# Optimization experiments

Measured on AMD Instinct MI355X. Metric: run time of the kernel, lower is better.

The kernel has to match this reference:

```python
import jax, jax.numpy as jnp
import numpy as np

B, N, D, H = 4, 4096, 64, 128
N_STATES = 6
K = 10  # top-k nearest neighbors in detect_basins
EPS = 1e-12


def setup_inputs() -> dict:
    key = jax.random.key(0)
    ks = jax.random.split(key, 12)
    s = 0.05
    return {
        "conformations": jax.random.normal(ks[0], (B, N, D), dtype=jnp.float32),
        "native_state": jax.random.normal(ks[1], (B, D), dtype=jnp.float32),
        # energy net: D -> H -> H//2 -> 1
        "We1": jax.random.normal(ks[2], (D, H), dtype=jnp.float32) * s,
        "be1": jnp.zeros((H,), jnp.float32),
        "We2": jax.random.normal(ks[3], (H, H // 2), dtype=jnp.float32) * s,
        "be2": jnp.zeros((H // 2,), jnp.float32),
        "We3": jax.random.normal(ks[4], (H // 2, 1), dtype=jnp.float32) * s,
        "be3": jnp.zeros((1,), jnp.float32),
        # state classifier: D -> H -> 6
        "Ws1": jax.random.normal(ks[5], (D, H), dtype=jnp.float32) * s,
        "bs1": jnp.zeros((H,), jnp.float32),
        "Ws2": jax.random.normal(ks[6], (H, N_STATES), dtype=jnp.float32) * s,
        "bs2": jnp.zeros((N_STATES,), jnp.float32),
    }


def reference(conformations, native_state, We1, be1, We2, be2, We3, be3, Ws1, bs1, Ws2, bs2):
    relu = jax.nn.relu

    def analyze(conf, native):  # conf: (N, D), native: (D,)
        # predict_energy
        h = relu(conf @ We1 + be1)
        h = relu(h @ We2 + be2)
        e = (h @ We3 + be3)[:, 0]  # (N,)

        # detect_basins: pairwise euclidean distances via Gram trick
        sq = jnp.sum(conf * conf, axis=-1)  # (N,)
        d2 = sq[:, None] + sq[None, :] - 2.0 * (conf @ conf.T)
        dist = jnp.sqrt(jnp.clip(d2, EPS))  # (N, N); eps keeps sqrt grad finite at diag

        negv, idx = jax.lax.top_k(-dist, K)   # ascending distances; idx[:,0] == self
        r = -negv[:, -1]                      # k-th smallest distance per row
        neigh_e = e[idx[:, 1:]]               # (N, K-1) energies of 9 nearest neighbors
        is_basin = jnp.all(e[:, None] <= neigh_e, axis=1)  # local-minimum test

        mask = dist < r[:, None]              # points strictly inside basin radius (incl self)
        depth = jnp.max(jnp.where(mask, e[None, :], -jnp.inf), axis=1) - e
        width = jnp.sum(jnp.where(mask, dist, 0.0), axis=1) / jnp.sum(mask, axis=1)

        # classify_state (computed for every sample; original queries it per basin center)
        logits = relu(conf @ Ws1 + bs1) @ Ws2 + bs2  # (N, 6)

        # compute_funnel_metrics
        nd = jnp.sqrt(jnp.sum((conf - native) ** 2, axis=-1))  # (N,)
        native_energy = e[jnp.argmin(nd)]
        funnel_depth = jnp.max(e) - native_energy
        ruggedness = jnp.std(e, ddof=1)  # torch.std is unbiased
        corr = jnp.corrcoef(jnp.stack([nd, e]))[0, 1]
        se = e[jnp.argsort(nd)]
        frustration = jnp.mean((se[1:] > se[:-1]).astype(jnp.float32))
        metrics = jnp.stack([funnel_depth, ruggedness, corr, frustration, native_energy])
        return e, is_basin, depth, width, logits, metrics

    return jax.vmap(analyze)(conformations, native_state)
```

## Files before the change

kernel.cpp:

```cpp
#include <hip/hip_runtime.h>
#include <float.h>
#include <math.h>

#define NPTS 4096
#define NBATCH 4
#define BN (NBATCH * NPTS)
#define EPSC 1e-12f
#define JS 4
#define CSTRIDE 204
#define NT (NPTS / JS / 64)

typedef __attribute__((ext_vector_type(8))) short bfrag;
typedef __attribute__((ext_vector_type(4))) short bhalf;
typedef __attribute__((ext_vector_type(4))) float f32x4;

#define MFMA(A, B, C) __builtin_amdgcn_mfma_f32_16x16x32_bf16((A), (B), (C), 0, 0, 0)

__device__ __forceinline__ bool dless(float d1, int i1, float d2, int i2) {
  return (d1 < d2) || ((d1 == d2) && (i1 < i2));
}

__device__ __forceinline__ unsigned short f2bf(float x) {
  unsigned b = __float_as_uint(x);
  return (unsigned short)((b + 0x7FFFu + ((b >> 16) & 1u)) >> 16);
}
__device__ __forceinline__ float bf2f(unsigned short u) {
  return __uint_as_float(((unsigned)u) << 16);
}
__device__ __forceinline__ void bf3(float x, unsigned short& u0, unsigned short& u1,
                                    unsigned short& u2) {
  u0 = f2bf(x);
  float r = x - bf2f(u0);
  u1 = f2bf(r);
  r = r - bf2f(u1);
  u2 = f2bf(r);
}

__device__ __forceinline__ void cp16(const void* g, void* l) {
  __builtin_amdgcn_global_load_lds(
      (const __attribute__((address_space(1))) unsigned int*)g,
      (__attribute__((address_space(3))) unsigned int*)l, 16, 0, 0);
}
__device__ __forceinline__ void cp4(const void* g, void* l) {
  __builtin_amdgcn_global_load_lds(
      (const __attribute__((address_space(1))) unsigned int*)g,
      (__attribute__((address_space(3))) unsigned int*)l, 4, 0, 0);
}

__device__ __forceinline__ void gemm32x128(const float (*A)[64], const float* W,
                                           const float* bias, float (*O)[128], int tid) {
  const int pi = (tid >> 5) << 2;
  const int ci = (tid & 31) << 2;
  float acc[4][4] = {};
  for (int k0 = 0; k0 < 64; k0 += 4) {
    alignas(16) float av[4][4], wv[4][4];
#pragma unroll
    for (int r = 0; r < 4; ++r) *(float4*)av[r] = *(const float4*)&A[pi + r][k0];
#pragma unroll
    for (int kk = 0; kk < 4; ++kk) *(float4*)wv[kk] = *(const float4*)&W[(k0 + kk) * 128 + ci];
#pragma unroll
    for (int kk = 0; kk < 4; ++kk)
#pragma unroll
      for (int r = 0; r < 4; ++r)
#pragma unroll
        for (int c = 0; c < 4; ++c)
          acc[r][c] = fmaf(av[r][kk], wv[kk][c], acc[r][c]);
  }
#pragma unroll
  for (int r = 0; r < 4; ++r)
#pragma unroll
    for (int c = 0; c < 4; ++c)
      O[pi + r][ci + c] = fmaxf(acc[r][c] + bias[ci + c], 0.f);
}

__global__ __launch_bounds__(256) void mlp_kernel(
    const float* __restrict__ conf, const float* __restrict__ native,
    const float* __restrict__ We1, const float* __restrict__ be1,
    const float* __restrict__ We2, const float* __restrict__ be2,
    const float* __restrict__ We3, const float* __restrict__ be3,
    const float* __restrict__ Ws1, const float* __restrict__ bs1,
    const float* __restrict__ Ws2, const float* __restrict__ bs2,
    float* __restrict__ e_out, float* __restrict__ logits_out,
    float* __restrict__ sq_ws, float* __restrict__ nd_ws,
    unsigned short* __restrict__ cbf) {
  __shared__ __align__(16) float Wbuf[8192];
  __shared__ __align__(16) float confs[32][64];
  __shared__ __align__(16) float hbuf[32][128];
  __shared__ float nat[64];
  __shared__ float b1s[128], b2s[64], w3s[64], bs1s[128], ws2s[768], bs2s[6];
  __shared__ float be3s;

  const int tid = threadIdx.x;
  const int blk = blockIdx.x;
  const int b = blk >> 7;
  const int pbase = (blk & 127) * 32;
  const float* confb = conf + ((size_t)b * NPTS + pbase) * 64;

  for (int q = tid; q < 512; q += 256) {
    float4 v = *(const float4*)(confb + q * 4);
    *(float4*)&confs[q >> 4][(q & 15) << 2] = v;
  }
  if (tid < 64) nat[tid] = native[b * 64 + tid];
  if (tid < 128) b1s[tid] = be1[tid];
  if (tid < 64) b2s[tid] = be2[tid];
  if (tid < 64) w3s[tid] = We3[tid];
  if (tid < 128) bs1s[tid] = bs1[tid];
  for (int q = tid; q < 768; q += 256) ws2s[q] = Ws2[q];
  if (tid < 6) bs2s[tid] = bs2[tid];
  if (tid == 0) be3s = be3[0];
  for (int q = tid; q < 2048; q += 256)
    *(float4*)&Wbuf[q * 4] = *(const float4*)(Ws1 + q * 4);
  __syncthreads();

  for (int q = tid; q < 512; q += 256) {
    const int pl = q >> 4, k4 = (q & 15) << 2;
    float4 v = *(const float4*)&confs[pl][k4];
    unsigned short x0, x1, x2, y0, y1, y2, z0, z1, z2, w0, w1, w2;
    bf3(v.x, x0, x1, x2);
    bf3(v.y, y0, y1, y2);
    bf3(v.z, z0, z1, z2);
    bf3(v.w, w0, w1, w2);
    unsigned short* dst = cbf + (size_t)(b * NPTS + pbase + pl) * CSTRIDE + k4;
    *(bhalf*)&dst[0] = (bhalf){(short)x0, (short)y0, (short)z0, (short)w0};
    *(bhalf*)&dst[64] = (bhalf){(short)x1, (short)y1, (short)z1, (short)w1};
    *(bhalf*)&dst[128] = (bhalf){(short)x2, (short)y2, (short)z2, (short)w2};
  }

  if (tid < 32) {
    float rs_[8], rn_[8];
#pragma unroll
    for (int u = 0; u < 8; ++u) {
      float c = confs[tid][u];
      rs_[u] = c * c;
      float d = c - nat[u];
      rn_[u] = d * d;
    }
    for (int d0 = 8; d0 < 64; d0 += 8) {
#pragma unroll
      for (int u = 0; u < 8; ++u) {
        float c = confs[tid][d0 + u];
        rs_[u] += c * c;
        float d = c - nat[d0 + u];
        rn_[u] += d * d;
      }
    }
    float s = ((rs_[0] + rs_[1]) + (rs_[2] + rs_[3])) + ((rs_[4] + rs_[5]) + (rs_[6] + rs_[7]));
    float n = ((rn_[0] + rn_[1]) + (rn_[2] + rn_[3])) + ((rn_[4] + rn_[5]) + (rn_[6] + rn_[7]));
    sq_ws[(size_t)b * NPTS + pbase + tid] = s;
    nd_ws[(size_t)b * NPTS + pbase + tid] = sqrtf(n);
  }

  gemm32x128(confs, Wbuf, bs1s, hbuf, tid);
  __syncthreads();

  for (int q = tid; q < 2048; q += 256)
    *(float4*)&Wbuf[q * 4] = *(const float4*)(We1 + q * 4);
  if (tid < 192) {
    int p = tid / 6, s = tid % 6;
    float acc = 0.f;
#pragma unroll 8
    for (int h = 0; h < 128; ++h)
      acc = fmaf(hbuf[p][h], ws2s[h * 6 + s], acc);
    logits_out[((size_t)b * NPTS + pbase + p) * 6 + s] = acc + bs2s[s];
  }
  __syncthreads();

  gemm32x128(confs, Wbuf, b1s, hbuf, tid);
  __syncthreads();

  for (int q = tid; q < 2048; q += 256)
    *(float4*)&Wbuf[q * 4] = *(const float4*)(We2 + q * 4);
  __syncthreads();

  if (tid < 128) {
    const int pi = (tid >> 4) << 2;
    const int ci = (tid & 15) << 2;
    float acc[4][4] = {};
    for (int k0 = 0; k0 < 128; k0 += 4) {
      alignas(16) float av[4][4], wv[4][4];
#pragma unroll
      for (int r = 0; r < 4; ++r) *(float4*)av[r] = *(const float4*)&hbuf[pi + r][k0];
#pragma unroll
      for (int kk = 0; kk < 4; ++kk) *(float4*)wv[kk] = *(const float4*)&Wbuf[(k0 + kk) * 64 + ci];
#pragma unroll
      for (int kk = 0; kk < 4; ++kk)
#pragma unroll
        for (int r = 0; r < 4; ++r)
#pragma unroll
          for (int c = 0; c < 4; ++c)
            acc[r][c] = fmaf(av[r][kk], wv[kk][c], acc[r][c]);
    }
#pragma unroll
    for (int r = 0; r < 4; ++r)
#pragma unroll
      for (int c = 0; c < 4; ++c)
        confs[pi + r][ci + c] = fmaxf(acc[r][c] + b2s[ci + c], 0.f);
  }
  __syncthreads();

  if (tid < 32) {
    float acc = 0.f;
#pragma unroll
    for (int k = 0; k < 64; ++k)
      acc = fmaf(confs[tid][k], w3s[k], acc);
    e_out[(size_t)b * NPTS + pbase + tid] = acc + be3s;
  }
}

__device__ __forceinline__ bfrag ldfrag(const unsigned short* p) {
  bhalf lo = *(const bhalf*)p;
  bhalf hi = *(const bhalf*)(p + 4);
  return __builtin_shufflevector(lo, hi, 0, 1, 2, 3, 4, 5, 6, 7);
}

__device__ __forceinline__ void stage_async(const unsigned short* src,
                                            unsigned short* BU,
                                            const float* sqsrc, float* sqjs,
                                            int tid) {
  const char* s = (const char*)src;
  char* d = (char*)BU;
#pragma unroll
  for (int it = 0; it < 6; ++it) {
    const int q = it * 256 + tid;
    cp16(s + (size_t)q * 16, d + (size_t)q * 16);
  }
  if (tid < 96) {
    const int q = 1536 + tid;
    cp16(s + (size_t)q * 16, d + (size_t)q * 16);
  }
  if (tid < 64) cp4(sqsrc + tid, sqjs + tid);
}

__global__ __launch_bounds__(256, 1) void topk_part_kernel(
    const unsigned short* __restrict__ cbf, const float* __restrict__ sq_ws,
    float* __restrict__ topd, unsigned short* __restrict__ topi) {
  __shared__ __align__(16) unsigned short BU[64 * CSTRIDE];
  __shared__ __align__(16) float Dsf[64 * 68];
  __shared__ float sqjs[64];

  const int tid = threadIdx.x;
  const int b = blockIdx.z;
  const int i0 = blockIdx.x * 64;
  const int jbase = blockIdx.y * (NPTS / JS);
  const unsigned short* cbfb = cbf + (size_t)b * NPTS * CSTRIDE;
  const float* sqb = sq_ws + (size_t)b * NPTS;

  const int l = tid & 63, w = tid >> 6;
  const int cl = l & 15, g = l >> 4;

  const unsigned short* arow = cbfb + (size_t)(i0 + 16 * w + cl) * CSTRIDE + g * 8;
  const bfrag a00 = ldfrag(arow + 0);
  const bfrag a01 = ldfrag(arow + 32);
  const bfrag a10 = ldfrag(arow + 64);
  const bfrag a11 = ldfrag(arow + 96);
  const bfrag a20 = ldfrag(arow + 128);
  const bfrag a21 = ldfrag(arow + 160);
  float sqar[4];
#pragma unroll
  for (int e = 0; e < 4; ++e) sqar[e] = sqb[i0 + 16 * w + 4 * g + e];

  const int irow = tid >> 2, q4 = tid & 3;

  unsigned long long lk[10];
#pragma unroll
  for (int k = 0; k < 10; ++k) lk[k] = 0x7F7FFFFF7FFFFFFFULL;
  float thrf = FLT_MAX;

  stage_async(cbfb + (size_t)jbase * CSTRIDE, BU, sqb + jbase, sqjs, tid);
  __syncthreads();

  for (int jt = 0; jt < NT; ++jt) {
    const int j0 = jbase + jt * 64;

#pragma unroll
    for (int c2 = 0; c2 < 2; ++c2) {
      const unsigned short* bpA = &BU[(32 * c2 + cl) * CSTRIDE + g * 8];
      const unsigned short* bpB = &BU[(32 * c2 + 16 + cl) * CSTRIDE + g * 8];
      const bfrag bA00 = ldfrag(bpA + 0);
      const bfrag bA01 = ldfrag(bpA + 32);
      const bfrag bA10 = ldfrag(bpA + 64);
      const bfrag bA11 = ldfrag(bpA + 96);
      const bfrag bA20 = ldfrag(bpA + 128);
      const bfrag bA21 = ldfrag(bpA + 160);
      const bfrag bB00 = ldfrag(bpB + 0);
      const bfrag bB01 = ldfrag(bpB + 32);
      const bfrag bB10 = ldfrag(bpB + 64);
      const bfrag bB11 = ldfrag(bpB + 96);
      const bfrag bB20 = ldfrag(bpB + 128);
      const bfrag bB21 = ldfrag(bpB + 160);
      f32x4 accA = {0.f, 0.f, 0.f, 0.f};
      f32x4 accB = {0.f, 0.f, 0.f, 0.f};
      accA = MFMA(a00, bA00, accA); accB = MFMA(a00, bB00, accB);
      accA = MFMA(a01, bA01, accA); accB = MFMA(a01, bB01, accB);
      accA = MFMA(a00, bA10, accA); accB = MFMA(a00, bB10, accB);
      accA = MFMA(a01, bA11, accA); accB = MFMA(a01, bB11, accB);
      accA = MFMA(a10, bA00, accA); accB = MFMA(a10, bB00, accB);
      accA = MFMA(a11, bA01, accA); accB = MFMA(a11, bB01, accB);
      accA = MFMA(a00, bA20, accA); accB = MFMA(a00, bB20, accB);
      accA = MFMA(a01, bA21, accA); accB = MFMA(a01, bB21, accB);
      accA = MFMA(a10, bA10, accA); accB = MFMA(a10, bB10, accB);
      accA = MFMA(a11, bA11, accA); accB = MFMA(a11, bB11, accB);
      accA = MFMA(a20, bA00, accA); accB = MFMA(a20, bB00, accB);
      accA = MFMA(a21, bA01, accA); accB = MFMA(a21, bB01, accB);
      const int colA = 32 * c2 + cl;
      const int colB = colA + 16;
      const float sjA = sqjs[colA];
      const float sjB = sqjs[colB];
#pragma unroll
      for (int e = 0; e < 4; ++e) {
        const int rw = 16 * w + 4 * g + e;
        float d2A = fmaf(-2.f, accA[e], sqar[e] + sjA);
        float d2B = fmaf(-2.f, accB[e], sqar[e] + sjB);
        Dsf[rw * 68 + colA] = fmaxf(d2A, EPSC);
        Dsf[rw * 68 + colB] = fmaxf(d2B, EPSC);
      }
    }
    __syncthreads();

    if (jt + 1 < NT)
      stage_async(cbfb + (size_t)(j0 + 64) * CSTRIDE, BU, sqb + j0 + 64, sqjs, tid);

    const float* drow = &Dsf[irow * 68 + q4 * 16];
    unsigned mask = 0;
#pragma unroll
    for (int cc = 0; cc < 4; ++cc) {
      float4 v = *(const float4*)&drow[cc * 4];
      mask |= (v.x <= thrf) ? (1u << (cc * 4 + 0)) : 0u;
      mask |= (v.y <= thrf) ? (1u << (cc * 4 + 1)) : 0u;
      mask |= (v.z <= thrf) ? (1u << (cc * 4 + 2)) : 0u;
      mask |= (v.w <= thrf) ? (1u << (cc * 4 + 3)) : 0u;
    }
    const int cnt = __popc(mask);
    int K = cnt;
#pragma unroll
    for (int off = 32; off >= 1; off >>= 1) K = max(K, __shfl_xor(K, off, 64));

    int id = (__ffs(mask) - 1) & 15;
    mask &= mask - 1;
    float dcur = drow[id];
    int jcur = j0 + q4 * 16 + id;
    for (int k = 0; k < K; ++k) {
      const int idn = (__ffs(mask) - 1) & 15;
      mask &= mask - 1;
      const float dnx = drow[idn];
      const int jnx = j0 + q4 * 16 + idn;
      if (k < cnt) {
        unsigned long long cur =
            (((unsigned long long)__float_as_uint(dcur)) << 32) |
            (unsigned long long)(unsigned)jcur;
        if (cur < lk[9]) {
#pragma unroll
          for (int kk = 0; kk < 10; ++kk) {
            bool lt = cur < lk[kk];
            unsigned long long mn = lt ? cur : lk[kk];
            cur = lt ? lk[kk] : cur;
            lk[kk] = mn;
          }
        }
      }
      dcur = dnx;
      jcur = jnx;
    }

    float t = __uint_as_float((unsigned)(lk[9] >> 32));
    t = fminf(t, __shfl_xor(t, 1, 4));
    t = fminf(t, __shfl_xor(t, 2, 4));
    thrf = t;
    __syncthreads();
  }

  float* mrgD = Dsf;
  int* mrgI = (int*)BU;
  {
#pragma unroll
    for (int k = 0; k < 10; ++k) {
      mrgD[irow * 40 + q4 * 10 + k] = __uint_as_float((unsigned)(lk[k] >> 32));
      mrgI[irow * 40 + q4 * 10 + k] = (int)(unsigned)(lk[k] & 0xFFFFFFFFu);
    }
  }
  __syncthreads();
  if (tid < 64) {
    const int base = tid * 40;
    int h0 = 0, h1 = 0, h2 = 0, h3 = 0;
    const size_t obase = (((size_t)b * NPTS + i0 + tid) * JS + blockIdx.y) * 10;
    for (int k = 0; k < 10; ++k) {
      float bd = FLT_MAX; int bi = 0x7fffffff; int bl = -1;
      { float d = mrgD[base + h0];      int ii = mrgI[base + h0];      if (dless(d, ii, bd, bi)) { bd = d; bi = ii; bl = 0; } }
      { float d = mrgD[base + 10 + h1]; int ii = mrgI[base + 10 + h1]; if (dless(d, ii, bd, bi)) { bd = d; bi = ii; bl = 1; } }
      { float d = mrgD[base + 20 + h2]; int ii = mrgI[base + 20 + h2]; if (dless(d, ii, bd, bi)) { bd = d; bi = ii; bl = 2; } }
      { float d = mrgD[base + 30 + h3]; int ii = mrgI[base + 30 + h3]; if (dless(d, ii, bd, bi)) { bd = d; bi = ii; bl = 3; } }
      h0 += (bl == 0); h1 += (bl == 1); h2 += (bl == 2); h3 += (bl == 3);
      topd[obase + k] = bd;
      topi[obase + k] = (unsigned short)bi;
    }
  }
}

__global__ __launch_bounds__(256) void merge_rank_kernel(
    const float* __restrict__ topd, const unsigned short* __restrict__ topi,
    const float* __restrict__ e_in, const float* __restrict__ nd_ws,
    float* __restrict__ basin_out, float* __restrict__ depth_out,
    float* __restrict__ width_out, float* __restrict__ se_ws) {
  __shared__ __align__(16) float ndl[4096];
  const int tid = threadIdx.x;
  if (blockIdx.x < 64) {
    const int g = blockIdx.x * 256 + tid;
    const int b = g >> 12;
    const float* eb = e_in + (size_t)b * NPTS;
    const float* td = topd + (size_t)g * (JS * 10);
    const unsigned short* ti = topi + (size_t)g * (JS * 10);
    const float e_i = eb[g & (NPTS - 1)];
    int h0 = 0, h1 = 0, h2 = 0, h3 = 0;
    float dk[10];
    int ik[10];
#pragma unroll
    for (int k = 0; k < 10; ++k) {
      float bd = FLT_MAX; int bi = 0x7fffffff; int bl = -1;
      { float d = td[h0];      int ii = ti[h0];      if (dless(d, ii, bd, bi)) { bd = d; bi = ii; bl = 0; } }
      { float d = td[10 + h1]; int ii = ti[10 + h1]; if (dless(d, ii, bd, bi)) { bd = d; bi = ii; bl = 1; } }
      { float d = td[20 + h2]; int ii = ti[20 + h2]; if (dless(d, ii, bd, bi)) { bd = d; bi = ii; bl = 2; } }
      { float d = td[30 + h3]; int ii = ti[30 + h3]; if (dless(d, ii, bd, bi)) { bd = d; bi = ii; bl = 3; } }
      h0 += (bl == 0); h1 += (bl == 1); h2 += (bl == 2); h3 += (bl == 3);
      dk[k] = bd;
      ik[k] = bi;
    }
    const float r2 = dk[9];
    bool basin = true;
    float mx = -FLT_MAX, sum = 0.f, cnt = 0.f;
#pragma unroll
    for (int k = 0; k < 10; ++k) {
      float ev = eb[ik[k]];
      if (dk[k] < r2) { mx = fmaxf(mx, ev); sum += sqrtf(dk[k]); cnt += 1.f; }
      if (k >= 1) basin = basin && (e_i <= ev);
    }
    basin_out[g] = basin ? 1.f : 0.f;
    depth_out[g] = mx - e_i;
    width_out[g] = sum / cnt;
  } else {
    const int rb = blockIdx.x - 64;
    const int b = rb >> 6;
    const int i0 = (rb & 63) * 64;
    const float* ndb = nd_ws + (size_t)b * NPTS;
    for (int q = tid; q < 1024; q += 256)
      *(float4*)&ndl[q * 4] = *(const float4*)(ndb + q * 4);
    __syncthreads();
    const int i = i0 + (tid >> 2);
    const int qp = tid & 3;
    const float ndi = ndl[i];
    int rank = 0;
    for (int j = qp * 1024; j < qp * 1024 + 1024; j += 4) {
      float4 v = *(const float4*)&ndl[j];
      rank += (v.x < ndi) || (v.x == ndi && (j + 0) < i);
      rank += (v.y < ndi) || (v.y == ndi && (j + 1) < i);
      rank += (v.z < ndi) || (v.z == ndi && (j + 2) < i);
      rank += (v.w < ndi) || (v.w == ndi && (j + 3) < i);
    }
    rank += __shfl_xor(rank, 1, 4);
    rank += __shfl_xor(rank, 2, 4);
    if (qp == 0) se_ws[(size_t)b * NPTS + rank] = e_in[(size_t)b * NPTS + i];
  }
}

__device__ __forceinline__ float wave_sum(float v) {
#pragma unroll
  for (int off = 32; off >= 1; off >>= 1) v += __shfl_xor(v, off, 64);
  return v;
}
__device__ __forceinline__ float wave_max(float v) {
#pragma unroll
  for (int off = 32; off >= 1; off >>= 1) v = fmaxf(v, __shfl_xor(v, off, 64));
  return v;
}

__global__ __launch_bounds__(1024) void metrics_kernel(
    const float* __restrict__ e_in, const float* __restrict__ nd_ws,
    const float* __restrict__ se_ws, float* __restrict__ metrics_out) {
  __shared__ __align__(16) float el[4096], ndl[4096], sel[4096];
  __shared__ float rA[16], rB[16], rC[16], rD[16], rE[16], rV[16];
  __shared__ int rI[16];
  const int tid = threadIdx.x;
  const int b = blockIdx.x;
  const int wid = tid >> 6, ln = tid & 63;
  const float* eb = e_in + (size_t)b * NPTS;
  const float* ndb = nd_ws + (size_t)b * NPTS;
  const float* seb = se_ws + (size_t)b * NPTS;
  *(float4*)&el[tid * 4] = *(const float4*)(eb + tid * 4);
  *(float4*)&ndl[tid * 4] = *(const float4*)(ndb + tid * 4);
  *(float4*)&sel[tid * 4] = *(const float4*)(seb + tid * 4);
  __syncthreads();

  float pe = 0.f, pnd = 0.f;
  for (int p = tid; p < 4096; p += 1024) { pe += el[p]; pnd += ndl[p]; }
  pe = wave_sum(pe);
  pnd = wave_sum(pnd);
  if (ln == 0) { rA[wid] = pe; rB[wid] = pnd; }
  __syncthreads();
  float me = 0.f, mnd = 0.f;
  for (int i = 0; i < 16; ++i) { me += rA[i]; mnd += rB[i]; }
  me /= 4096.f;
  mnd /= 4096.f;
  __syncthreads();

  float sxx = 0.f, syy = 0.f, sxy = 0.f, mx = -FLT_MAX;
  float bestv = FLT_MAX;
  int besti = 0x7fffffff;
  for (int p = tid; p < 4096; p += 1024) {
    float de = el[p] - me, dn = ndl[p] - mnd;
    syy += de * de;
    sxx += dn * dn;
    sxy += de * dn;
    mx = fmaxf(mx, el[p]);
    if (ndl[p] < bestv || (ndl[p] == bestv && p < besti)) { bestv = ndl[p]; besti = p; }
  }
  float fr = 0.f;
  for (int p = tid; p < 4095; p += 1024) fr += (sel[p + 1] > sel[p]) ? 1.f : 0.f;

  sxx = wave_sum(sxx);
  syy = wave_sum(syy);
  sxy = wave_sum(sxy);
  mx = wave_max(mx);
  fr = wave_sum(fr);
#pragma unroll
  for (int off = 32; off >= 1; off >>= 1) {
    float ov = __shfl_xor(bestv, off, 64);
    int oi = __shfl_xor(besti, off, 64);
    if (ov < bestv || (ov == bestv && oi < besti)) { bestv = ov; besti = oi; }
  }
  if (ln == 0) {
    rA[wid] = sxx; rB[wid] = syy; rC[wid] = sxy;
    rD[wid] = mx;  rE[wid] = fr;  rV[wid] = bestv; rI[wid] = besti;
  }
  __syncthreads();
  if (tid == 0) {
    float tsxx = 0.f, tsyy = 0.f, tsxy = 0.f, tmx = -FLT_MAX, tfr = 0.f;
    float bv = FLT_MAX;
    int bi = 0x7fffffff;
    for (int i = 0; i < 16; ++i) {
      tsxx += rA[i]; tsyy += rB[i]; tsxy += rC[i];
      tmx = fmaxf(tmx, rD[i]); tfr += rE[i];
      if (rV[i] < bv || (rV[i] == bv && rI[i] < bi)) { bv = rV[i]; bi = rI[i]; }
    }
    float ne = el[bi];
    metrics_out[b * 5 + 0] = tmx - ne;
    metrics_out[b * 5 + 1] = sqrtf(tsyy / 4095.f);
    metrics_out[b * 5 + 2] = tsxy / sqrtf(tsxx * tsyy);
    metrics_out[b * 5 + 3] = tfr / 4095.f;
    metrics_out[b * 5 + 4] = ne;
  }
}

extern "C" void kernel_launch(void* const* d_in, const int* in_sizes, int n_in,
                              void* d_out, int out_size, void* d_ws, size_t ws_size,
                              hipStream_t stream) {
  const float* conf = (const float*)d_in[0];
  const float* native = (const float*)d_in[1];
  const float* We1 = (const float*)d_in[2];
  const float* be1 = (const float*)d_in[3];
  const float* We2 = (const float*)d_in[4];
  const float* be2 = (const float*)d_in[5];
  const float* We3 = (const float*)d_in[6];
  const float* be3 = (const float*)d_in[7];
  const float* Ws1 = (const float*)d_in[8];
  const float* bs1 = (const float*)d_in[9];
  const float* Ws2 = (const float*)d_in[10];
  const float* bs2 = (const float*)d_in[11];

  float* out = (float*)d_out;
  float* e_out = out;
  float* basin_out = out + BN;
  float* depth_out = out + 2 * BN;
  float* width_out = out + 3 * BN;
  float* logits_out = out + 4 * BN;
  float* metrics_out = out + 10 * BN;

  float* wsf = (float*)d_ws;
  float* sq_ws = wsf;
  float* nd_ws = wsf + BN;
  float* se_ws = wsf + 2 * (size_t)BN;
  float* topd = wsf + 3 * (size_t)BN;
  unsigned short* topi = (unsigned short*)(wsf + 43 * (size_t)BN);
  unsigned short* cbf = (unsigned short*)(wsf + 63 * (size_t)BN);

  mlp_kernel<<<dim3(512), dim3(256), 0, stream>>>(
      conf, native, We1, be1, We2, be2, We3, be3, Ws1, bs1, Ws2, bs2,
      e_out, logits_out, sq_ws, nd_ws, cbf);
  topk_part_kernel<<<dim3(64, JS, NBATCH), dim3(256), 0, stream>>>(
      cbf, sq_ws, topd, topi);
  merge_rank_kernel<<<dim3(320), dim3(256), 0, stream>>>(
      topd, topi, e_out, nd_ws, basin_out, depth_out, width_out, se_ws);
  metrics_kernel<<<dim3(NBATCH), dim3(1024), 0, stream>>>(e_out, nd_ws, se_ws, metrics_out);
}
```

Measured before the change: 201.5 us.

## Store bf16 split conformations in MFMA-fragment tiled layout and load B directly from global

Changes the bf16x3 split conformation workspace from a padded row-major layout to a layout tiled per 16 points, so each lane's 8-element MFMA fragment is one contiguous 16-byte load. The top-k kernel drops its LDS staging buffer and async global-to-LDS copies, reading A and B fragments and squared norms straight from global memory. This removes LDS traffic and shrinks shared memory use. In exchange there is no prefetch overlap, and every wave issues its own global loads for the shared B tile, which relies on L1/L2 hits and exposes global latency before each MFMA chain.

```diff
diff --git a/kernel.cpp b/kernel.cpp
--- a/kernel.cpp
+++ b/kernel.cpp
@@ -7,8 +7,9 @@
 #define BN (NBATCH * NPTS)
 #define EPSC 1e-12f
 #define JS 4
-#define CSTRIDE 204
 #define NT (NPTS / JS / 64)
+#define T16US 3072
+#define BATCHUS 786432
 
 typedef __attribute__((ext_vector_type(8))) short bfrag;
 typedef __attribute__((ext_vector_type(4))) short bhalf;
@@ -34,17 +35,6 @@
   u1 = f2bf(r);
   r = r - bf2f(u1);
   u2 = f2bf(r);
-}
-
-__device__ __forceinline__ void cp16(const void* g, void* l) {
-  __builtin_amdgcn_global_load_lds(
-      (const __attribute__((address_space(1))) unsigned int*)g,
-      (__attribute__((address_space(3))) unsigned int*)l, 16, 0, 0);
-}
-__device__ __forceinline__ void cp4(const void* g, void* l) {
-  __builtin_amdgcn_global_load_lds(
-      (const __attribute__((address_space(1))) unsigned int*)g,
-      (__attribute__((address_space(3))) unsigned int*)l, 4, 0, 0);
 }
 
 __device__ __forceinline__ void gemm32x128(const float (*A)[64], const float* W,
@@ -120,10 +110,16 @@
     bf3(v.y, y0, y1, y2);
     bf3(v.z, z0, z1, z2);
     bf3(v.w, w0, w1, w2);
-    unsigned short* dst = cbf + (size_t)(b * NPTS + pbase + pl) * CSTRIDE + k4;
-    *(bhalf*)&dst[0] = (bhalf){(short)x0, (short)y0, (short)z0, (short)w0};
-    *(bhalf*)&dst[64] = (bhalf){(short)x1, (short)y1, (short)z1, (short)w1};
-    *(bhalf*)&dst[128] = (bhalf){(short)x2, (short)y2, (short)z2, (short)w2};
+    const int pt = pbase + pl;
+    const int t16 = pt >> 4, r = pt & 15;
+    const int h = k4 >> 5;
+    const int kp = k4 & 31;
+    const int g = kp >> 3, off = kp & 7;
+    unsigned short* base = cbf + (size_t)b * BATCHUS + (size_t)t16 * T16US +
+                           h * 512 + g * 128 + r * 8 + off;
+    *(bhalf*)(base + 0) = (bhalf){(short)x0, (short)y0, (short)z0, (short)w0};
+    *(bhalf*)(base + 1024) = (bhalf){(short)x1, (short)y1, (short)z1, (short)w1};
+    *(bhalf*)(base + 2048) = (bhalf){(short)x2, (short)y2, (short)z2, (short)w2};
   }
 
   if (tid < 32) {
@@ -207,54 +203,30 @@
   }
 }
 
-__device__ __forceinline__ bfrag ldfrag(const unsigned short* p) {
-  bhalf lo = *(const bhalf*)p;
-  bhalf hi = *(const bhalf*)(p + 4);
-  return __builtin_shufflevector(lo, hi, 0, 1, 2, 3, 4, 5, 6, 7);
-}
-
-__device__ __forceinline__ void stage_async(const unsigned short* src,
-                                            unsigned short* BU,
-                                            const float* sqsrc, float* sqjs,
-                                            int tid) {
-  const char* s = (const char*)src;
-  char* d = (char*)BU;
-#pragma unroll
-  for (int it = 0; it < 6; ++it) {
-    const int q = it * 256 + tid;
-    cp16(s + (size_t)q * 16, d + (size_t)q * 16);
-  }
-  if (tid < 96) {
-    const int q = 1536 + tid;
-    cp16(s + (size_t)q * 16, d + (size_t)q * 16);
-  }
-  if (tid < 64) cp4(sqsrc + tid, sqjs + tid);
-}
-
 __global__ __launch_bounds__(256, 1) void topk_part_kernel(
     const unsigned short* __restrict__ cbf, const float* __restrict__ sq_ws,
     float* __restrict__ topd, unsigned short* __restrict__ topi) {
-  __shared__ __align__(16) unsigned short BU[64 * CSTRIDE];
   __shared__ __align__(16) float Dsf[64 * 68];
-  __shared__ float sqjs[64];
+  __shared__ __align__(16) int mrgI_s[2560];
 
   const int tid = threadIdx.x;
   const int b = blockIdx.z;
   const int i0 = blockIdx.x * 64;
   const int jbase = blockIdx.y * (NPTS / JS);
-  const unsigned short* cbfb = cbf + (size_t)b * NPTS * CSTRIDE;
+  const unsigned short* cbfb = cbf + (size_t)b * BATCHUS;
   const float* sqb = sq_ws + (size_t)b * NPTS;
 
   const int l = tid & 63, w = tid >> 6;
   const int cl = l & 15, g = l >> 4;
 
-  const unsigned short* arow = cbfb + (size_t)(i0 + 16 * w + cl) * CSTRIDE + g * 8;
-  const bfrag a00 = ldfrag(arow + 0);
-  const bfrag a01 = ldfrag(arow + 32);
-  const bfrag a10 = ldfrag(arow + 64);
-  const bfrag a11 = ldfrag(arow + 96);
-  const bfrag a20 = ldfrag(arow + 128);
-  const bfrag a21 = ldfrag(arow + 160);
+  const unsigned short* abase =
+      cbfb + (size_t)(i0 / 16 + w) * T16US + (size_t)l * 8;
+  const bfrag a00 = *(const bfrag*)(abase + 0);
+  const bfrag a01 = *(const bfrag*)(abase + 512);
+  const bfrag a10 = *(const bfrag*)(abase + 1024);
+  const bfrag a11 = *(const bfrag*)(abase + 1536);
+  const bfrag a20 = *(const bfrag*)(abase + 2048);
+  const bfrag a21 = *(const bfrag*)(abase + 2560);
   float sqar[4];
 #pragma unroll
   for (int e = 0; e < 4; ++e) sqar[e] = sqb[i0 + 16 * w + 4 * g + e];
@@ -266,28 +238,26 @@
   for (int k = 0; k < 10; ++k) lk[k] = 0x7F7FFFFF7FFFFFFFULL;
   float thrf = FLT_MAX;
 
-  stage_async(cbfb + (size_t)jbase * CSTRIDE, BU, sqb + jbase, sqjs, tid);
-  __syncthreads();
-
   for (int jt = 0; jt < NT; ++jt) {
     const int j0 = jbase + jt * 64;
 
 #pragma unroll
     for (int c2 = 0; c2 < 2; ++c2) {
-      const unsigned short* bpA = &BU[(32 * c2 + cl) * CSTRIDE + g * 8];
-      const unsigned short* bpB = &BU[(32 * c2 + 16 + cl) * CSTRIDE + g * 8];
-      const bfrag bA00 = ldfrag(bpA + 0);
-      const bfrag bA01 = ldfrag(bpA + 32);
-      const bfrag bA10 = ldfrag(bpA + 64);
-      const bfrag bA11 = ldfrag(bpA + 96);
-      const bfrag bA20 = ldfrag(bpA + 128);
-      const bfrag bA21 = ldfrag(bpA + 160);
-      const bfrag bB00 = ldfrag(bpB + 0);
-      const bfrag bB01 = ldfrag(bpB + 32);
-      const bfrag bB10 = ldfrag(bpB + 64);
-      const bfrag bB11 = ldfrag(bpB + 96);
-      const bfrag bB20 = ldfrag(bpB + 128);
-      const bfrag bB21 = ldfrag(bpB + 160);
+      const unsigned short* bbA =
+          cbfb + (size_t)(j0 / 16 + 2 * c2) * T16US + (size_t)l * 8;
+      const unsigned short* bbB = bbA + T16US;
+      const bfrag bA00 = *(const bfrag*)(bbA + 0);
+      const bfrag bA01 = *(const bfrag*)(bbA + 512);
+      const bfrag bA10 = *(const bfrag*)(bbA + 1024);
+      const bfrag bA11 = *(const bfrag*)(bbA + 1536);
+      const bfrag bA20 = *(const bfrag*)(bbA + 2048);
+      const bfrag bA21 = *(const bfrag*)(bbA + 2560);
+      const bfrag bB00 = *(const bfrag*)(bbB + 0);
+      const bfrag bB01 = *(const bfrag*)(bbB + 512);
+      const bfrag bB10 = *(const bfrag*)(bbB + 1024);
+      const bfrag bB11 = *(const bfrag*)(bbB + 1536);
+      const bfrag bB20 = *(const bfrag*)(bbB + 2048);
+      const bfrag bB21 = *(const bfrag*)(bbB + 2560);
       f32x4 accA = {0.f, 0.f, 0.f, 0.f};
       f32x4 accB = {0.f, 0.f, 0.f, 0.f};
       accA = MFMA(a00, bA00, accA); accB = MFMA(a00, bB00, accB);
@@ -304,8 +274,8 @@
       accA = MFMA(a21, bA01, accA); accB = MFMA(a21, bB01, accB);
       const int colA = 32 * c2 + cl;
       const int colB = colA + 16;
-      const float sjA = sqjs[colA];
-      const float sjB = sqjs[colB];
+      const float sjA = sqb[j0 + colA];
+      const float sjB = sqb[j0 + colB];
 #pragma unroll
       for (int e = 0; e < 4; ++e) {
         const int rw = 16 * w + 4 * g + e;
@@ -316,9 +286,6 @@
       }
     }
     __syncthreads();
-
-    if (jt + 1 < NT)
-      stage_async(cbfb + (size_t)(j0 + 64) * CSTRIDE, BU, sqb + j0 + 64, sqjs, tid);
 
     const float* drow = &Dsf[irow * 68 + q4 * 16];
     unsigned mask = 0;
@@ -370,7 +337,7 @@
   }
 
   float* mrgD = Dsf;
-  int* mrgI = (int*)BU;
+  int* mrgI = mrgI_s;
   {
 #pragma unroll
     for (int k = 0; k < 10; ++k) {
```

Result: slower. 223.5 us (+10.9%).
